# Kernel tuning notes

Measured on AMD Instinct MI355X. Metric: run time of the kernel, lower is better.

The kernel has to match this reference:

```python
import jax, jax.numpy as jnp
import numpy as np

K_SIZE = 25  # fixed blur kernel size, covers 3*sigma_max (sigma_max=4 -> 2*ceil(12)+1=25)


def _forward(x, sigma_u, glare_u, occ_u, rain_u, rain_n_u, rain_alpha_u,
             noise_u, noise_amt_u, apply_flags):
    B, C, H, W = x.shape
    dt = x.dtype
    yy = jnp.arange(H, dtype=dt)[:, None]   # [H,1]
    xx = jnp.arange(W, dtype=dt)[None, :]   # [1,W]

    def gate(i, new, old):
        f = (apply_flags[:, i] > 0)[:, None, None, None]
        return jnp.where(f, new, old)

    out = x

    # ---- 1. GaussianBlur: per-sample sigma in (1,4), separable depthwise conv ----
    half = K_SIZE // 2
    sigma = 1.0 + 3.0 * sigma_u                                  # [B]
    coords = jnp.arange(K_SIZE, dtype=dt) - half                 # [K]
    g = jnp.exp(-coords[None, :] ** 2 / (2.0 * sigma[:, None] ** 2))
    g = g / g.sum(axis=1, keepdims=True)                         # [B,K]
    kern_h = jnp.broadcast_to(g[:, None, :], (B, C, K_SIZE)).reshape(B * C, 1, 1, K_SIZE)
    dn = ('NCHW', 'OIHW', 'NCHW')
    xb = out.reshape(1, B * C, H, W)
    xb = jax.lax.conv_general_dilated(xb, kern_h, (1, 1), ((0, 0), (half, half)),
                                      dimension_numbers=dn, feature_group_count=B * C)
    kern_v = kern_h.transpose(0, 1, 3, 2)                        # [BC,1,K,1]
    xb = jax.lax.conv_general_dilated(xb, kern_v, (1, 1), ((half, half), (0, 0)),
                                      dimension_numbers=dn, feature_group_count=B * C)
    blurred = jnp.clip(xb.reshape(B, C, H, W), 0.0, 1.0)
    out = gate(0, blurred, out)

    # ---- 2. GlareOverlay: additive anisotropic gaussian blob ----
    intensity = 0.4 + 0.5 * glare_u[:, 0]
    rx = (0.1 + 0.25 * glare_u[:, 1]) * W / 2
    ry = (0.1 + 0.25 * glare_u[:, 2]) * H / 2
    cx = (0.2 + 0.6 * glare_u[:, 3]) * W
    cy = (0.2 + 0.6 * glare_u[:, 4]) * H
    e = lambda v: v[:, None, None]  # [B] -> [B,1,1]
    gmask = jnp.exp(-(((xx[None] - e(cx)) / e(rx)) ** 2 + ((yy[None] - e(cy)) / e(ry)) ** 2))
    glared = jnp.clip(out + (intensity[:, None, None] * gmask)[:, None], 0.0, 1.0)
    out = gate(1, glared, out)

    # ---- 3. OcclusionPatch: rectangle filled with 0 ----
    ph = jnp.floor(H * (0.1 + 0.3 * occ_u[:, 0]))
    pw = jnp.floor(W * (0.1 + 0.3 * occ_u[:, 1]))
    y0 = jnp.floor(occ_u[:, 2] * (H - ph))
    x0 = jnp.floor(occ_u[:, 3] * (W - pw))
    omask = ((yy[None] >= e(y0)) & (yy[None] < e(y0 + ph)) &
             (xx[None] >= e(x0)) & (xx[None] < e(x0 + pw)))      # [B,H,W]
    occluded = jnp.where(omask[:, None], jnp.zeros((), dt), out)
    out = gate(2, occluded, out)

    # ---- 4. RainStreaks: up to 60 two-pixel-wide vertical streaks, alpha-compounded ----
    S = rain_u.shape[1]
    n = jnp.floor(20.0 + 41.0 * rain_n_u)                        # [B] in [20,60]
    a = 0.15 + 0.35 * rain_alpha_u                               # [B]
    xc = jnp.floor(rain_u[:, :, 0] * W)                          # [B,S]
    y0s = jnp.floor(rain_u[:, :, 1] * (H // 2))
    y1s = (H // 2) + jnp.floor(rain_u[:, :, 2] * (H // 2))
    hh = jnp.arange(H, dtype=dt)[None, None, :]                  # [1,1,H]
    ww = jnp.arange(W, dtype=dt)[None, None, :]                  # [1,1,W]
    rowm = ((hh >= y0s[:, :, None]) & (hh < y1s[:, :, None])).astype(dt)   # [B,S,H]
    colm = ((ww >= xc[:, :, None] - 1) & (ww <= xc[:, :, None])).astype(dt)  # [B,S,W]
    active = (jnp.arange(S, dtype=dt)[None, :] < n[:, None]).astype(dt)    # [B,S]
    count = jnp.einsum('bsh,bsw->bhw', rowm * active[:, :, None], colm)    # overlap counts
    decay = (1.0 - a)[:, None, None, None] ** count[:, None]     # (1-a)^c
    rained = jnp.clip(out * decay + (1.0 - decay), 0.0, 1.0)
    out = gate(3, rained, out)

    # ---- 5. SaltPepperNoise ----
    amount = (0.01 + 0.07 * noise_amt_u)[:, None, None, None]
    noisy = jnp.where(noise_u < amount / 2, jnp.zeros((), dt),
                      jnp.where(noise_u > 1.0 - amount / 2, jnp.ones((), dt), out))
    out = gate(4, noisy, out)

    return out


def setup_inputs() -> dict:
    key = jax.random.key(0)
    ks = jax.random.split(key, 10)
    B, C, H, W = 32, 3, 512, 512
    u = lambda k, shape: jax.random.uniform(k, shape, dtype=jnp.float32)
    return {
        'x': u(ks[0], (B, C, H, W)),
        'sigma_u': u(ks[1], (B,)),
        'glare_u': u(ks[2], (B, 5)),
        'occ_u': u(ks[3], (B, 4)),
        'rain_u': u(ks[4], (B, 60, 3)),
        'rain_n_u': u(ks[5], (B,)),
        'rain_alpha_u': u(ks[6], (B,)),
        'noise_u': u(ks[7], (B, C, H, W)),
        'noise_amt_u': u(ks[8], (B,)),
        'apply_flags': jax.random.randint(ks[9], (B, 5), 0, 2, dtype=jnp.int32),
    }


def reference(x, sigma_u, glare_u, occ_u, rain_u, rain_n_u, rain_alpha_u,
              noise_u, noise_amt_u, apply_flags):
    return _forward(x, sigma_u, glare_u, occ_u, rain_u, rain_n_u, rain_alpha_u,
                    noise_u, noise_amt_u, apply_flags)
```

## Files before the change

kernel.cpp:

```cpp
#include <hip/hip_runtime.h>

#define NB   32
#define NC   3
#define NH   512
#define NW   512
#define KS   25
#define HALF 12
#define NS   60
#define PLN  (NH * NW)
#define NPL  (NB * NC)

typedef _Float16 half4 __attribute__((ext_vector_type(4)));
typedef _Float16 half8 __attribute__((ext_vector_type(8)));

#define HB_BYTES  ((size_t)NPL * PLN * 2)
#define WTS_OFF   HB_BYTES
#define WTS_BYTES ((size_t)4096)
#define NL_OFF    (WTS_OFF + WTS_BYTES)
#define NL_BYTES  ((size_t)NB * NW * 4)
#define PK_OFF    (NL_OFF + NL_BYTES)
#define PK_BYTES  ((size_t)NB * NW * NS * 4)
#define WS_NEED   (PK_OFF + PK_BYTES)

__device__ __forceinline__ float clip01(float v) { return fminf(fmaxf(v, 0.f), 1.f); }

struct PParams {
  int f1, f2, f3, f4;
  float intensity, cx, cy, rxi, ryi;
  float oy0, oy1, ox0, ox1;
  float log1ma;
  float thr_lo, thr_hi;
};

__device__ __forceinline__ PParams load_params(
    int b, const int* __restrict__ flags, const float* __restrict__ glare_u,
    const float* __restrict__ occ_u, const float* __restrict__ rain_alpha_u,
    const float* __restrict__ noise_amt_u)
{
  PParams P;
  P.f1 = flags[b * 5 + 1] > 0;
  P.f2 = flags[b * 5 + 2] > 0;
  P.f3 = flags[b * 5 + 3] > 0;
  P.f4 = flags[b * 5 + 4] > 0;
  float g0 = glare_u[b * 5 + 0], g1 = glare_u[b * 5 + 1], g2 = glare_u[b * 5 + 2],
        g3 = glare_u[b * 5 + 3], g4 = glare_u[b * 5 + 4];
  P.intensity = 0.4f + 0.5f * g0;
  P.rxi = 1.f / ((0.1f + 0.25f * g1) * 256.f);
  P.ryi = 1.f / ((0.1f + 0.25f * g2) * 256.f);
  P.cx = (0.2f + 0.6f * g3) * 512.f;
  P.cy = (0.2f + 0.6f * g4) * 512.f;
  float o0 = occ_u[b * 4 + 0], o1 = occ_u[b * 4 + 1],
        o2 = occ_u[b * 4 + 2], o3 = occ_u[b * 4 + 3];
  float ph = floorf(512.f * (0.1f + 0.3f * o0));
  float pw = floorf(512.f * (0.1f + 0.3f * o1));
  P.oy0 = floorf(o2 * (512.f - ph)); P.oy1 = P.oy0 + ph;
  P.ox0 = floorf(o3 * (512.f - pw)); P.ox1 = P.ox0 + pw;
  P.log1ma = log2f(1.f - (0.15f + 0.35f * rain_alpha_u[b]));
  float half_amt = 0.5f * (0.01f + 0.07f * noise_amt_u[b]);
  P.thr_lo = half_amt; P.thr_hi = 1.f - half_amt;
  return P;
}

__global__ void prep_kernel(const float* __restrict__ rain_u,
                            const float* __restrict__ rain_n_u,
                            const float* __restrict__ sigma_u,
                            int* __restrict__ nlist,
                            unsigned* __restrict__ packed,
                            float* __restrict__ wts)
{
  if (blockIdx.x == 64) {
    int b = threadIdx.x;
    if (b < NB) {
      float sig = 1.f + 3.f * sigma_u[b];
      float ninv = -1.f / (2.f * sig * sig);
      float w[KS]; float s = 0.f;
      #pragma unroll
      for (int j = 0; j < KS; ++j) {
        float d = (float)j - 12.f;
        w[j] = __expf(d * d * ninv);
        s += w[j];
      }
      float inv = 1.f / s;
      #pragma unroll
      for (int j = 0; j < KS; ++j) wts[b * 28 + j] = w[j] * inv;
    }
    return;
  }
  int t = blockIdx.x * 256 + threadIdx.x;
  if (t >= NB * NW) return;
  int b = t >> 9, wcol = t & 511;
  float n = floorf(20.f + 41.f * rain_n_u[b]);
  float wf = (float)wcol;
  int cnt = 0;
  for (int s = 0; s < NS; ++s) {
    if ((float)s < n) {
      float xc = floorf(rain_u[(b * NS + s) * 3 + 0] * 512.f);
      if (wf >= xc - 1.f && wf <= xc) {
        float y0 = floorf(rain_u[(b * NS + s) * 3 + 1] * 256.f);
        float y1 = 256.f + floorf(rain_u[(b * NS + s) * 3 + 2] * 256.f);
        packed[t * NS + cnt] = (((unsigned)y0) << 16) | (unsigned)y1;
        ++cnt;
      }
    }
  }
  nlist[t] = cnt;
}

template<int KR>
__device__ __forceinline__ void chain_quadN(
    float (&a)[KR][4], const PParams& P, int b, int gx0, int gy0,
    const float* __restrict__ np_plane, const int* __restrict__ nlist,
    const unsigned* __restrict__ packed, float* __restrict__ op_plane)
{
  if (P.f1) {
    float dx2[4];
    #pragma unroll
    for (int c = 0; c < 4; ++c) {
      float dx = ((float)(gx0 + c) - P.cx) * P.rxi;
      dx2[c] = dx * dx;
    }
    #pragma unroll
    for (int k = 0; k < KR; ++k) {
      float dy = ((float)(gy0 + k) - P.cy) * P.ryi;
      float dy2 = dy * dy;
      #pragma unroll
      for (int c = 0; c < 4; ++c) {
        float g = __expf(-(dx2[c] + dy2));
        a[k][c] = clip01(a[k][c] + P.intensity * g);
      }
    }
  }
  if (P.f2) {
    #pragma unroll
    for (int c = 0; c < 4; ++c) {
      float fx = (float)(gx0 + c);
      if (fx >= P.ox0 && fx < P.ox1) {
        #pragma unroll
        for (int k = 0; k < KR; ++k) {
          float fy = (float)(gy0 + k);
          if (fy >= P.oy0 && fy < P.oy1) a[k][c] = 0.f;
        }
      }
    }
  }
  if (P.f3) {
    #pragma unroll
    for (int c = 0; c < 4; ++c) {
      int base = b * NW + gx0 + c;
      int n = nlist[base];
      if (n > 0) {
        float cnt[KR];
        #pragma unroll
        for (int k = 0; k < KR; ++k) cnt[k] = 0.f;
        for (int j = 0; j < n; ++j) {
          unsigned p = packed[base * NS + j];
          float y0 = (float)(p >> 16), y1 = (float)(p & 0xffffu);
          #pragma unroll
          for (int k = 0; k < KR; ++k) {
            float fy = (float)(gy0 + k);
            cnt[k] += (fy >= y0 && fy < y1) ? 1.f : 0.f;
          }
        }
        #pragma unroll
        for (int k = 0; k < KR; ++k) {
          if (cnt[k] != 0.f) {
            float d = exp2f(cnt[k] * P.log1ma);
            a[k][c] = clip01(a[k][c] * d + (1.f - d));
          }
        }
      }
    }
  }
  if (P.f4) {
    #pragma unroll
    for (int k = 0; k < KR; ++k) {
      float4 nv = *reinterpret_cast<const float4*>(
          np_plane + (size_t)(gy0 + k) * NW + gx0);
      a[k][0] = (nv.x < P.thr_lo) ? 0.f : ((nv.x > P.thr_hi) ? 1.f : a[k][0]);
      a[k][1] = (nv.y < P.thr_lo) ? 0.f : ((nv.y > P.thr_hi) ? 1.f : a[k][1]);
      a[k][2] = (nv.z < P.thr_lo) ? 0.f : ((nv.z > P.thr_hi) ? 1.f : a[k][2]);
      a[k][3] = (nv.w < P.thr_lo) ? 0.f : ((nv.w > P.thr_hi) ? 1.f : a[k][3]);
    }
  }
  #pragma unroll
  for (int k = 0; k < KR; ++k)
    *reinterpret_cast<float4*>(op_plane + (size_t)(gy0 + k) * NW + gx0) =
        make_float4(a[k][0], a[k][1], a[k][2], a[k][3]);
}

__global__ __launch_bounds__(256, 4)
void k1_kernel(const float* __restrict__ x, const int* __restrict__ flags,
               const float* __restrict__ wts,
               const float* __restrict__ glare_u, const float* __restrict__ occ_u,
               const float* __restrict__ rain_alpha_u,
               const float* __restrict__ noise_u, const float* __restrict__ noise_amt_u,
               const int* __restrict__ nlist, const unsigned* __restrict__ packed,
               _Float16* __restrict__ hb, float* __restrict__ out)
{
  const int b = blockIdx.z, ch = blockIdx.y;
  const int tid = threadIdx.x;
  const int r0 = blockIdx.x << 3;
  const size_t plane = (size_t)(b * NC + ch) * PLN;

  if (flags[b * 5] > 0) {
    float w[KS];
    const float* wp = wts + b * 28;
    #pragma unroll
    for (int j = 0; j < KS; ++j) w[j] = wp[j];

    const int lane = tid & 63, wv = tid >> 6;
    const int wstart = (lane << 3) - HALF;

    #pragma unroll
    for (int rr = 0; rr < 2; ++rr) {
      const int row = r0 + wv + (rr << 2);
      const float* rowp = x + plane + (size_t)row * NW;

      float win[44];
      #pragma unroll
      for (int j = 0; j < 11; ++j) {
        int col = wstart + 4 * j;
        col = max(0, min(col, NW - 4));
        float4 v = *reinterpret_cast<const float4*>(rowp + col);
        win[4 * j + 0] = v.x; win[4 * j + 1] = v.y;
        win[4 * j + 2] = v.z; win[4 * j + 3] = v.w;
      }
      if (lane == 0) {
        #pragma unroll
        for (int i = 0; i < 12; ++i) win[i] = 0.f;
      }
      if (lane == 1) {
        #pragma unroll
        for (int i = 0; i < 4; ++i) win[i] = 0.f;
      }
      if (lane == 62) {
        #pragma unroll
        for (int i = 28; i < 44; ++i) win[i] = 0.f;
      }
      if (lane == 63) {
        #pragma unroll
        for (int i = 20; i < 44; ++i) win[i] = 0.f;
      }

      float acc[8];
      #pragma unroll
      for (int e = 0; e < 8; ++e) acc[e] = 0.f;
      #pragma unroll
      for (int t = 0; t < KS; ++t) {
        float wt = w[t];
        #pragma unroll
        for (int e = 0; e < 8; ++e) acc[e] = fmaf(wt, win[t + e], acc[e]);
      }
      half8 o;
      #pragma unroll
      for (int e = 0; e < 8; ++e) o[e] = (_Float16)acc[e];
      *reinterpret_cast<half8*>(hb + plane + (size_t)row * NW + (lane << 3)) = o;
    }
  } else {
    PParams P = load_params(b, flags, glare_u, occ_u, rain_alpha_u, noise_amt_u);
    const int gx0 = (tid & 127) << 2;
    const int gy0 = r0 + ((tid >> 7) << 2);
    float a[4][4];
    const float* xp = x + plane + gx0;
    #pragma unroll
    for (int k = 0; k < 4; ++k) {
      float4 v = *reinterpret_cast<const float4*>(xp + (size_t)(gy0 + k) * NW);
      a[k][0] = v.x; a[k][1] = v.y; a[k][2] = v.z; a[k][3] = v.w;
    }
    chain_quadN<4>(a, P, b, gx0, gy0, noise_u + plane, nlist, packed, out + plane);
  }
}

__global__ __launch_bounds__(256, 4)
void k2_kernel(const _Float16* __restrict__ hb, const float* __restrict__ wts,
               const float* __restrict__ glare_u, const float* __restrict__ occ_u,
               const float* __restrict__ rain_alpha_u,
               const float* __restrict__ noise_u, const float* __restrict__ noise_amt_u,
               const int* __restrict__ flags,
               const int* __restrict__ nlist, const unsigned* __restrict__ packed,
               float* __restrict__ out)
{
  const int lb = blockIdx.x;
  const int xcd = lb & 7, j = lb >> 3;
  const int pl = j >> 2, sub = j & 3;
  const int grp = (xcd + pl) & 7;
  const int strip = (grp << 2) | sub;
  const int b = pl / 3;
  if (flags[b * 5] <= 0) return;

  const int tid = threadIdx.x;
  const int gy0 = strip * 16 + ((tid >> 7) << 3);
  const int gx0 = (tid & 127) << 2;
  PParams P = load_params(b, flags, glare_u, occ_u, rain_alpha_u, noise_amt_u);
  const size_t plane = (size_t)pl * PLN;

  float w[KS];
  const float* wp = wts + b * 28;
  #pragma unroll
  for (int jj = 0; jj < KS; ++jj) w[jj] = wp[jj];

  float a[8][4];
  #pragma unroll
  for (int k = 0; k < 8; ++k) {
    a[k][0] = 0.f; a[k][1] = 0.f; a[k][2] = 0.f; a[k][3] = 0.f;
  }
  if (gy0 >= 16 && gy0 <= 488) {
    const _Float16* hp0 = hb + plane + (size_t)(gy0 - HALF) * NW + gx0;
    #pragma unroll
    for (int m = 0; m < 32; ++m) {
      half4 v = *reinterpret_cast<const half4*>(hp0 + (size_t)m * NW);
      float v0 = (float)v.x, v1 = (float)v.y, v2 = (float)v.z, v3 = (float)v.w;
      #pragma unroll
      for (int k = 0; k < 8; ++k) {
        int wi = m - k;
        if (wi >= 0 && wi <= 24) {
          float wt = w[wi];
          a[k][0] = fmaf(wt, v0, a[k][0]);
          a[k][1] = fmaf(wt, v1, a[k][1]);
          a[k][2] = fmaf(wt, v2, a[k][2]);
          a[k][3] = fmaf(wt, v3, a[k][3]);
        }
      }
    }
  } else {
    const _Float16* hp = hb + plane + gx0;
    #pragma unroll
    for (int m = 0; m < 32; ++m) {
      int gy = gy0 - HALF + m;
      if ((unsigned)gy < (unsigned)NH) {
        half4 v = *reinterpret_cast<const half4*>(hp + (size_t)gy * NW);
        float v0 = (float)v.x, v1 = (float)v.y, v2 = (float)v.z, v3 = (float)v.w;
        #pragma unroll
        for (int k = 0; k < 8; ++k) {
          int wi = m - k;
          if (wi >= 0 && wi <= 24) {
            float wt = w[wi];
            a[k][0] = fmaf(wt, v0, a[k][0]);
            a[k][1] = fmaf(wt, v1, a[k][1]);
            a[k][2] = fmaf(wt, v2, a[k][2]);
            a[k][3] = fmaf(wt, v3, a[k][3]);
          }
        }
      }
    }
  }
  #pragma unroll
  for (int k = 0; k < 8; ++k) {
    a[k][0] = clip01(a[k][0]); a[k][1] = clip01(a[k][1]);
    a[k][2] = clip01(a[k][2]); a[k][3] = clip01(a[k][3]);
  }
  chain_quadN<8>(a, P, b, gx0, gy0, noise_u + plane, nlist, packed, out + plane);
}

__global__ __launch_bounds__(256, 4)
void fallback_kernel(const float* __restrict__ x, const float* __restrict__ sigma_u,
                     const float* __restrict__ glare_u, const float* __restrict__ occ_u,
                     const float* __restrict__ rain_u, const float* __restrict__ rain_n_u,
                     const float* __restrict__ rain_alpha_u, const float* __restrict__ noise_u,
                     const float* __restrict__ noise_amt_u, const int* __restrict__ flags,
                     float* __restrict__ out)
{
  const int b = blockIdx.z, ch = blockIdx.y;
  const int ty0 = (blockIdx.x >> 3) * 64, tx0 = (blockIdx.x & 7) * 64;
  const int tid = threadIdx.x;
  const int f0 = flags[b * 5] > 0;
  PParams P = load_params(b, flags, glare_u, occ_u, rain_alpha_u, noise_amt_u);
  const float nrain = floorf(20.f + 41.f * rain_n_u[b]);
  const size_t plane = (size_t)(b * NC + ch) * PLN;
  const float* xp = x + plane;
  const float* np = noise_u + plane;
  float* op = out + plane;

  __shared__ __align__(16) float s_hb[88 * 64];

  float wr[KS];
  if (f0) {
    float sig = 1.f + 3.f * sigma_u[b];
    float ninv = -1.f / (2.f * sig * sig);
    float s = 0.f;
    #pragma unroll
    for (int t = 0; t < KS; ++t) {
      float d = (float)t - 12.f;
      wr[t] = __expf(d * d * ninv); s += wr[t];
    }
    float inv = 1.f / s;
    #pragma unroll
    for (int t = 0; t < KS; ++t) wr[t] *= inv;

    for (int i = tid; i < 88 * 16; i += 256) {
      int r = i >> 4, q = i & 15;
      int gy = ty0 + r - HALF;
      float a0 = 0.f, a1 = 0.f, a2 = 0.f, a3 = 0.f;
      if ((unsigned)gy < (unsigned)NH) {
        const float* rowp = xp + (size_t)gy * NW;
        int gx0 = tx0 + q * 4;
        float win[28];
        if (gx0 - HALF >= 0 && gx0 + 15 < NW) {
          #pragma unroll
          for (int j = 0; j < 7; ++j) {
            float4 v = *reinterpret_cast<const float4*>(rowp + gx0 - HALF + 4 * j);
            win[4 * j + 0] = v.x; win[4 * j + 1] = v.y;
            win[4 * j + 2] = v.z; win[4 * j + 3] = v.w;
          }
        } else {
          #pragma unroll
          for (int j = 0; j < 28; ++j) {
            int gx = gx0 - HALF + j;
            win[j] = ((unsigned)gx < (unsigned)NW) ? rowp[gx] : 0.f;
          }
        }
        #pragma unroll
        for (int t = 0; t < KS; ++t) {
          float wt = wr[t];
          a0 = fmaf(wt, win[t + 0], a0);
          a1 = fmaf(wt, win[t + 1], a1);
          a2 = fmaf(wt, win[t + 2], a2);
          a3 = fmaf(wt, win[t + 3], a3);
        }
      }
      *reinterpret_cast<float4*>(&s_hb[r * 64 + (i & 15) * 4]) =
          make_float4(a0, a1, a2, a3);
    }
    __syncthreads();
  }

  for (int i = tid; i < 512; i += 256) {
    int xq = i & 63, sy = i >> 6;
    int gx = tx0 + xq, gy0 = ty0 + sy * 8;
    float acc[8];
    if (f0) {
      float wincol[32];
      #pragma unroll
      for (int j = 0; j < 32; ++j) wincol[j] = s_hb[(sy * 8 + j) * 64 + xq];
      #pragma unroll
      for (int k = 0; k < 8; ++k) {
        float a = 0.f;
        #pragma unroll
        for (int t = 0; t < KS; ++t) a = fmaf(wr[t], wincol[k + t], a);
        acc[k] = clip01(a);
      }
    } else {
      #pragma unroll
      for (int k = 0; k < 8; ++k) acc[k] = xp[(size_t)(gy0 + k) * NW + gx];
    }
    const float fx = (float)gx;
    if (P.f1) {
      float dx = (fx - P.cx) * P.rxi;
      float dx2 = dx * dx;
      #pragma unroll
      for (int k = 0; k < 8; ++k) {
        float dy = ((float)(gy0 + k) - P.cy) * P.ryi;
        acc[k] = clip01(acc[k] + P.intensity * __expf(-(dx2 + dy * dy)));
      }
    }
    if (P.f2 && fx >= P.ox0 && fx < P.ox1) {
      #pragma unroll
      for (int k = 0; k < 8; ++k) {
        float fy = (float)(gy0 + k);
        if (fy >= P.oy0 && fy < P.oy1) acc[k] = 0.f;
      }
    }
    if (P.f3) {
      float cnt[8];
      #pragma unroll
      for (int k = 0; k < 8; ++k) cnt[k] = 0.f;
      for (int s = 0; s < NS; ++s) {
        if ((float)s < nrain) {
          float xc = floorf(rain_u[(b * NS + s) * 3 + 0] * 512.f);
          if (fx >= xc - 1.f && fx <= xc) {
            float y0 = floorf(rain_u[(b * NS + s) * 3 + 1] * 256.f);
            float y1 = 256.f + floorf(rain_u[(b * NS + s) * 3 + 2] * 256.f);
            #pragma unroll
            for (int k = 0; k < 8; ++k) {
              float fy = (float)(gy0 + k);
              cnt[k] += (fy >= y0 && fy < y1) ? 1.f : 0.f;
            }
          }
        }
      }
      #pragma unroll
      for (int k = 0; k < 8; ++k) {
        if (cnt[k] != 0.f) {
          float d = exp2f(cnt[k] * P.log1ma);
          acc[k] = clip01(acc[k] * d + (1.f - d));
        }
      }
    }
    if (P.f4) {
      #pragma unroll
      for (int k = 0; k < 8; ++k) {
        float nv = np[(size_t)(gy0 + k) * NW + gx];
        acc[k] = (nv < P.thr_lo) ? 0.f : ((nv > P.thr_hi) ? 1.f : acc[k]);
      }
    }
    #pragma unroll
    for (int k = 0; k < 8; ++k) op[(size_t)(gy0 + k) * NW + gx] = acc[k];
  }
}

extern "C" void kernel_launch(void* const* d_in, const int* in_sizes, int n_in,
                              void* d_out, int out_size, void* d_ws, size_t ws_size,
                              hipStream_t stream)
{
  const float* x            = (const float*)d_in[0];
  const float* sigma_u      = (const float*)d_in[1];
  const float* glare_u      = (const float*)d_in[2];
  const float* occ_u        = (const float*)d_in[3];
  const float* rain_u       = (const float*)d_in[4];
  const float* rain_n_u     = (const float*)d_in[5];
  const float* rain_alpha_u = (const float*)d_in[6];
  const float* noise_u      = (const float*)d_in[7];
  const float* noise_amt_u  = (const float*)d_in[8];
  const int*   flags        = (const int*)d_in[9];
  float* out = (float*)d_out;

  if (ws_size >= WS_NEED) {
    _Float16* hb     = (_Float16*)d_ws;
    float*    wts    = (float*)((char*)d_ws + WTS_OFF);
    int*      nlist  = (int*)((char*)d_ws + NL_OFF);
    unsigned* packed = (unsigned*)((char*)d_ws + PK_OFF);

    prep_kernel<<<65, 256, 0, stream>>>(rain_u, rain_n_u, sigma_u, nlist, packed, wts);
    k1_kernel<<<dim3(NH / 8, NC, NB), 256, 0, stream>>>(
        x, flags, wts, glare_u, occ_u, rain_alpha_u, noise_u, noise_amt_u,
        nlist, packed, hb, out);
    k2_kernel<<<3072, 256, 0, stream>>>(
        hb, wts, glare_u, occ_u, rain_alpha_u, noise_u, noise_amt_u,
        flags, nlist, packed, out);
  } else {
    dim3 grid(64, NC, NB);
    fallback_kernel<<<grid, 256, 0, stream>>>(
        x, sigma_u, glare_u, occ_u, rain_u, rain_n_u, rain_alpha_u,
        noise_u, noise_amt_u, flags, out);
  }
}
```

Measured before the change: 97.53 us.

## Fuse horizontal and vertical blur passes through shared-memory band buffer

Replaces the two-kernel blur (horizontal pass writing an fp16 plane to global workspace, then vertical pass) with one kernel. Each block computes a 16-row band's horizontal blur plus a 12-row halo on each side into LDS, then runs the vertical blur and the remaining chain from LDS. This removes the global intermediate round-trip and one launch. The cost is recomputing halo rows (40 rows per 16 output rows) and a 40KB LDS allocation that may cap occupancy.

```diff
diff --git a/kernel.cpp b/kernel.cpp
--- a/kernel.cpp
+++ b/kernel.cpp
@@ -9,12 +9,13 @@
 #define NS   60
 #define PLN  (NH * NW)
 #define NPL  (NB * NC)
+#define BAND 16
+#define HROWS (BAND + 2 * HALF)
 
 typedef _Float16 half4 __attribute__((ext_vector_type(4)));
 typedef _Float16 half8 __attribute__((ext_vector_type(8)));
 
-#define HB_BYTES  ((size_t)NPL * PLN * 2)
-#define WTS_OFF   HB_BYTES
+#define WTS_OFF   ((size_t)0)
 #define WTS_BYTES ((size_t)4096)
 #define NL_OFF    (WTS_OFF + WTS_BYTES)
 #define NL_BYTES  ((size_t)NB * NW * 4)
@@ -189,126 +190,103 @@
 }
 
 __global__ __launch_bounds__(256, 4)
-void k1_kernel(const float* __restrict__ x, const int* __restrict__ flags,
-               const float* __restrict__ wts,
-               const float* __restrict__ glare_u, const float* __restrict__ occ_u,
-               const float* __restrict__ rain_alpha_u,
-               const float* __restrict__ noise_u, const float* __restrict__ noise_amt_u,
-               const int* __restrict__ nlist, const unsigned* __restrict__ packed,
-               _Float16* __restrict__ hb, float* __restrict__ out)
-{
-  const int b = blockIdx.z, ch = blockIdx.y;
-  const int tid = threadIdx.x;
-  const int r0 = blockIdx.x << 3;
-  const size_t plane = (size_t)(b * NC + ch) * PLN;
-
-  if (flags[b * 5] > 0) {
-    float w[KS];
-    const float* wp = wts + b * 28;
-    #pragma unroll
-    for (int j = 0; j < KS; ++j) w[j] = wp[j];
-
-    const int lane = tid & 63, wv = tid >> 6;
-    const int wstart = (lane << 3) - HALF;
-
-    #pragma unroll
-    for (int rr = 0; rr < 2; ++rr) {
-      const int row = r0 + wv + (rr << 2);
-      const float* rowp = x + plane + (size_t)row * NW;
-
-      float win[44];
-      #pragma unroll
-      for (int j = 0; j < 11; ++j) {
-        int col = wstart + 4 * j;
-        col = max(0, min(col, NW - 4));
-        float4 v = *reinterpret_cast<const float4*>(rowp + col);
-        win[4 * j + 0] = v.x; win[4 * j + 1] = v.y;
-        win[4 * j + 2] = v.z; win[4 * j + 3] = v.w;
-      }
-      if (lane == 0) {
-        #pragma unroll
-        for (int i = 0; i < 12; ++i) win[i] = 0.f;
-      }
-      if (lane == 1) {
-        #pragma unroll
-        for (int i = 0; i < 4; ++i) win[i] = 0.f;
-      }
-      if (lane == 62) {
-        #pragma unroll
-        for (int i = 28; i < 44; ++i) win[i] = 0.f;
-      }
-      if (lane == 63) {
-        #pragma unroll
-        for (int i = 20; i < 44; ++i) win[i] = 0.f;
-      }
-
-      float acc[8];
-      #pragma unroll
-      for (int e = 0; e < 8; ++e) acc[e] = 0.f;
-      #pragma unroll
-      for (int t = 0; t < KS; ++t) {
-        float wt = w[t];
-        #pragma unroll
-        for (int e = 0; e < 8; ++e) acc[e] = fmaf(wt, win[t + e], acc[e]);
-      }
-      half8 o;
-      #pragma unroll
-      for (int e = 0; e < 8; ++e) o[e] = (_Float16)acc[e];
-      *reinterpret_cast<half8*>(hb + plane + (size_t)row * NW + (lane << 3)) = o;
-    }
-  } else {
-    PParams P = load_params(b, flags, glare_u, occ_u, rain_alpha_u, noise_amt_u);
-    const int gx0 = (tid & 127) << 2;
-    const int gy0 = r0 + ((tid >> 7) << 2);
-    float a[4][4];
-    const float* xp = x + plane + gx0;
-    #pragma unroll
-    for (int k = 0; k < 4; ++k) {
-      float4 v = *reinterpret_cast<const float4*>(xp + (size_t)(gy0 + k) * NW);
-      a[k][0] = v.x; a[k][1] = v.y; a[k][2] = v.z; a[k][3] = v.w;
-    }
-    chain_quadN<4>(a, P, b, gx0, gy0, noise_u + plane, nlist, packed, out + plane);
-  }
-}
-
-__global__ __launch_bounds__(256, 4)
-void k2_kernel(const _Float16* __restrict__ hb, const float* __restrict__ wts,
-               const float* __restrict__ glare_u, const float* __restrict__ occ_u,
-               const float* __restrict__ rain_alpha_u,
-               const float* __restrict__ noise_u, const float* __restrict__ noise_amt_u,
-               const int* __restrict__ flags,
-               const int* __restrict__ nlist, const unsigned* __restrict__ packed,
-               float* __restrict__ out)
+void fused_kernel(const float* __restrict__ x, const int* __restrict__ flags,
+                  const float* __restrict__ wts,
+                  const float* __restrict__ glare_u, const float* __restrict__ occ_u,
+                  const float* __restrict__ rain_alpha_u,
+                  const float* __restrict__ noise_u, const float* __restrict__ noise_amt_u,
+                  const int* __restrict__ nlist, const unsigned* __restrict__ packed,
+                  float* __restrict__ out)
 {
   const int lb = blockIdx.x;
   const int xcd = lb & 7, j = lb >> 3;
   const int pl = j >> 2, sub = j & 3;
   const int grp = (xcd + pl) & 7;
-  const int strip = (grp << 2) | sub;
+  const int band = (grp << 2) | sub;
   const int b = pl / 3;
-  if (flags[b * 5] <= 0) return;
-
+  const int y0 = band * BAND;
   const int tid = threadIdx.x;
-  const int gy0 = strip * 16 + ((tid >> 7) << 3);
-  const int gx0 = (tid & 127) << 2;
+  const size_t plane = (size_t)pl * PLN;
+
+  __shared__ __align__(16) _Float16 s_hb[HROWS * NW];
+
   PParams P = load_params(b, flags, glare_u, occ_u, rain_alpha_u, noise_amt_u);
-  const size_t plane = (size_t)pl * PLN;
-
-  float w[KS];
-  const float* wp = wts + b * 28;
-  #pragma unroll
-  for (int jj = 0; jj < KS; ++jj) w[jj] = wp[jj];
-
-  float a[8][4];
-  #pragma unroll
-  for (int k = 0; k < 8; ++k) {
-    a[k][0] = 0.f; a[k][1] = 0.f; a[k][2] = 0.f; a[k][3] = 0.f;
-  }
-  if (gy0 >= 16 && gy0 <= 488) {
-    const _Float16* hp0 = hb + plane + (size_t)(gy0 - HALF) * NW + gx0;
+
+  if (flags[b * 5] > 0) {
+    float w[KS];
+    const float* wp = wts + b * 28;
+    #pragma unroll
+    for (int jj = 0; jj < KS; ++jj) w[jj] = wp[jj];
+
+    const int lane = tid & 63, wv = tid >> 6;
+    const int wstart = (lane << 3) - HALF;
+
+    for (int k = 0; k < 10; ++k) {
+      const int i = wv + (k << 2);
+      const int hy = y0 - HALF + i;
+      half8 o;
+      if ((unsigned)hy < (unsigned)NH) {
+        const float* rowp = x + plane + (size_t)hy * NW;
+        float4 A[8];
+        #pragma unroll
+        for (int jj = 0; jj < 8; ++jj) {
+          int col = wstart + 4 * jj;
+          col = max(0, min(col, NW - 4));
+          A[jj] = *reinterpret_cast<const float4*>(rowp + col);
+        }
+        float win[32];
+        #pragma unroll
+        for (int jj = 0; jj < 8; ++jj) {
+          win[4 * jj + 0] = A[jj].x; win[4 * jj + 1] = A[jj].y;
+          win[4 * jj + 2] = A[jj].z; win[4 * jj + 3] = A[jj].w;
+        }
+        if (lane == 0) {
+          #pragma unroll
+          for (int ii = 0; ii < 12; ++ii) win[ii] = 0.f;
+        }
+        if (lane == 1) {
+          #pragma unroll
+          for (int ii = 0; ii < 4; ++ii) win[ii] = 0.f;
+        }
+        if (lane == 62) {
+          #pragma unroll
+          for (int ii = 28; ii < 32; ++ii) win[ii] = 0.f;
+        }
+        if (lane == 63) {
+          #pragma unroll
+          for (int ii = 20; ii < 32; ++ii) win[ii] = 0.f;
+        }
+        float acc[8];
+        #pragma unroll
+        for (int e = 0; e < 8; ++e) acc[e] = 0.f;
+        #pragma unroll
+        for (int t = 0; t < KS; ++t) {
+          float wt = w[t];
+          #pragma unroll
+          for (int e = 0; e < 8; ++e) acc[e] = fmaf(wt, win[t + e], acc[e]);
+        }
+        #pragma unroll
+        for (int e = 0; e < 8; ++e) o[e] = (_Float16)acc[e];
+      } else {
+        #pragma unroll
+        for (int e = 0; e < 8; ++e) o[e] = (_Float16)0.f;
+      }
+      *reinterpret_cast<half8*>(&s_hb[i * NW + (lane << 3)]) = o;
+    }
+    __syncthreads();
+
+    const int cq = tid & 127, rh = tid >> 7;
+    const int gx0 = cq << 2;
+    const int gy0 = y0 + (rh << 3);
+    float a[8][4];
+    #pragma unroll
+    for (int k = 0; k < 8; ++k) {
+      a[k][0] = 0.f; a[k][1] = 0.f; a[k][2] = 0.f; a[k][3] = 0.f;
+    }
     #pragma unroll
     for (int m = 0; m < 32; ++m) {
-      half4 v = *reinterpret_cast<const half4*>(hp0 + (size_t)m * NW);
+      const int i = (rh << 3) + m;
+      half4 v = *reinterpret_cast<const half4*>(&s_hb[i * NW + gx0]);
       float v0 = (float)v.x, v1 = (float)v.y, v2 = (float)v.z, v3 = (float)v.w;
       #pragma unroll
       for (int k = 0; k < 8; ++k) {
@@ -322,34 +300,25 @@
         }
       }
     }
+    #pragma unroll
+    for (int k = 0; k < 8; ++k) {
+      a[k][0] = clip01(a[k][0]); a[k][1] = clip01(a[k][1]);
+      a[k][2] = clip01(a[k][2]); a[k][3] = clip01(a[k][3]);
+    }
+    chain_quadN<8>(a, P, b, gx0, gy0, noise_u + plane, nlist, packed, out + plane);
   } else {
-    const _Float16* hp = hb + plane + gx0;
-    #pragma unroll
-    for (int m = 0; m < 32; ++m) {
-      int gy = gy0 - HALF + m;
-      if ((unsigned)gy < (unsigned)NH) {
-        half4 v = *reinterpret_cast<const half4*>(hp + (size_t)gy * NW);
-        float v0 = (float)v.x, v1 = (float)v.y, v2 = (float)v.z, v3 = (float)v.w;
-        #pragma unroll
-        for (int k = 0; k < 8; ++k) {
-          int wi = m - k;
-          if (wi >= 0 && wi <= 24) {
-            float wt = w[wi];
-            a[k][0] = fmaf(wt, v0, a[k][0]);
-            a[k][1] = fmaf(wt, v1, a[k][1]);
-            a[k][2] = fmaf(wt, v2, a[k][2]);
-            a[k][3] = fmaf(wt, v3, a[k][3]);
-          }
-        }
-      }
-    }
-  }
-  #pragma unroll
-  for (int k = 0; k < 8; ++k) {
-    a[k][0] = clip01(a[k][0]); a[k][1] = clip01(a[k][1]);
-    a[k][2] = clip01(a[k][2]); a[k][3] = clip01(a[k][3]);
-  }
-  chain_quadN<8>(a, P, b, gx0, gy0, noise_u + plane, nlist, packed, out + plane);
+    const int cq = tid & 127, rh = tid >> 7;
+    const int gx0 = cq << 2;
+    const int gy0 = y0 + (rh << 3);
+    float a[8][4];
+    const float* xp = x + plane + gx0;
+    #pragma unroll
+    for (int k = 0; k < 8; ++k) {
+      float4 v = *reinterpret_cast<const float4*>(xp + (size_t)(gy0 + k) * NW);
+      a[k][0] = v.x; a[k][1] = v.y; a[k][2] = v.z; a[k][3] = v.w;
+    }
+    chain_quadN<8>(a, P, b, gx0, gy0, noise_u + plane, nlist, packed, out + plane);
+  }
 }
 
 __global__ __launch_bounds__(256, 4)
@@ -515,18 +484,14 @@
   float* out = (float*)d_out;
 
   if (ws_size >= WS_NEED) {
-    _Float16* hb     = (_Float16*)d_ws;
     float*    wts    = (float*)((char*)d_ws + WTS_OFF);
     int*      nlist  = (int*)((char*)d_ws + NL_OFF);
     unsigned* packed = (unsigned*)((char*)d_ws + PK_OFF);
 
     prep_kernel<<<65, 256, 0, stream>>>(rain_u, rain_n_u, sigma_u, nlist, packed, wts);
-    k1_kernel<<<dim3(NH / 8, NC, NB), 256, 0, stream>>>(
+    fused_kernel<<<NPL * (NH / BAND), 256, 0, stream>>>(
         x, flags, wts, glare_u, occ_u, rain_alpha_u, noise_u, noise_amt_u,
-        nlist, packed, hb, out);
-    k2_kernel<<<3072, 256, 0, stream>>>(
-        hb, wts, glare_u, occ_u, rain_alpha_u, noise_u, noise_amt_u,
-        flags, nlist, packed, out);
+        nlist, packed, out);
   } else {
     dim3 grid(64, NC, NB);
     fallback_kernel<<<grid, 256, 0, stream>>>(
```

Result: no change. 97.22 us (-0.3%).
